# Kernel tuning notes

Measured on AMD Instinct MI355X. Metric: run time of the kernel, lower is better.

## Reference

```python
import jax, jax.numpy as jnp
import numpy as np

N_NODES = 10000
AVG_DEG = 32
N_FEAT = 512
HIDDEN = 32
CODE = 16


def setup_inputs() -> dict:
    key = jax.random.key(0)
    k1, k2, k3, k4, k5 = jax.random.split(key, 5)
    E = N_NODES * AVG_DEG
    src = jax.random.randint(k1, (E,), 0, N_NODES, dtype=jnp.int32)
    dst = jax.random.randint(k2, (E,), 0, N_NODES, dtype=jnp.int32)
    # A + I: add self loops (Kipf & Welling transform)
    loop = jnp.arange(N_NODES, dtype=jnp.int32)
    src = jnp.concatenate([src, loop])
    dst = jnp.concatenate([dst, loop])
    ones = jnp.ones(src.shape[0], jnp.float32)
    deg_row = jax.ops.segment_sum(ones, dst, num_segments=N_NODES)
    deg_col = jax.ops.segment_sum(ones, src, num_segments=N_NODES)
    # symmetric normalization D^-1/2 (A+I) D^-1/2
    edge_weight = jax.lax.rsqrt(deg_row[dst] * deg_col[src])
    x = jax.random.normal(k3, (N_NODES, N_FEAT), dtype=jnp.float32)
    W1 = jax.random.normal(k4, (N_FEAT, HIDDEN), dtype=jnp.float32) * 0.1
    W2 = jax.random.normal(k5, (HIDDEN, CODE), dtype=jnp.float32) * 0.1
    return {"x": x, "W1": W1, "W2": W2, "edge_weight": edge_weight,
            "src": src, "dst": dst}


def _spmm(edge_weight, src, dst, X):
    # sparse A_hat @ X via gather + weighted scatter-add
    return jax.ops.segment_sum(edge_weight[:, None] * X[src], dst,
                               num_segments=X.shape[0])


def reference(x, W1, W2, edge_weight, src, dst):
    # layer 1: A_hat @ (x @ W1), relu  (dropout inactive: eval mode)
    h = jax.nn.relu(_spmm(edge_weight, src, dst, x @ W1))
    # layer 2 (encoder): A_hat @ (h @ W2)
    z = _spmm(edge_weight, src, dst, h @ W2)  # [N, code]
    # inner-product decoder: sigmoid(Z Z^T)
    return jax.nn.sigmoid(jnp.einsum('nc,mc->nm', z, z))
```

## Files before the change

### kernel.cpp

```cpp
#include <hip/hip_runtime.h>
#include <hip/hip_bf16.h>

#define N_NODES 10000
#define N_FEAT  512
#define HIDDEN  32
#define CODE    16

typedef __attribute__((ext_vector_type(8))) short  short8;
typedef __attribute__((ext_vector_type(4))) float  floatx4;

__device__ __forceinline__ float bf2f(unsigned short h) {
    return __uint_as_float(((unsigned int)h) << 16);
}
__device__ __forceinline__ unsigned short f2bf(float f) {
    unsigned int u = __float_as_uint(f);
    u += 0x7fffu + ((u >> 16) & 1u);
    return (unsigned short)(u >> 16);
}
__device__ __forceinline__ float load_f(const void* p, size_t i, int isf32) {
    return isf32 ? ((const float*)p)[i] : bf2f(((const unsigned short*)p)[i]);
}
__device__ __forceinline__ int get_idx(const int* p, int e, int is64) {
    return is64 ? p[2 * (size_t)e] : p[e];
}

__global__ __launch_bounds__(384) void k_detect(const unsigned short* __restrict__ t0,
                                                const unsigned short* __restrict__ t1,
                                                const unsigned short* __restrict__ t2,
                                                const unsigned short* __restrict__ t3,
                                                const int* __restrict__ i0,
                                                const int* __restrict__ i1,
                                                int* __restrict__ flags) {
    const int w    = threadIdx.x >> 6;
    const int lane = threadIdx.x & 63;
    unsigned int m = 0;
    if (w < 4) {
        const unsigned short* p = (w == 0) ? t0 : (w == 1) ? t1 : (w == 2) ? t2 : t3;
        for (int i = lane; i < 128; i += 64) {
            unsigned int v = (unsigned int)p[2 * i] & 0x7fffu;
            m = m > v ? m : v;
        }
    } else {
        const int* p = (w == 4) ? i0 : i1;
        for (int i = lane; i < 128; i += 64) {
            m |= (unsigned int)p[2 * i + 1];
        }
    }
#pragma unroll
    for (int off = 32; off > 0; off >>= 1) {
        unsigned int o = (unsigned int)__shfl_down((int)m, off, 64);
        m = (w < 4) ? (m > o ? m : o) : (m | o);
    }
    if (lane == 0) flags[w] = (w < 4) ? (m >= 0x5000u ? 1 : 0) : (m == 0u ? 1 : 0);
}

__global__ __launch_bounds__(256) void k_xw1(const void* __restrict__ x,
                                             const void* __restrict__ W1,
                                             float* __restrict__ XW1,
                                             const int* __restrict__ flags) {
    const int xf32  = flags[0];
    const int w1f32 = flags[1];
    int t = blockIdx.x * 256 + threadIdx.x;
    if (t >= N_NODES * HIDDEN) return;
    const int n = t >> 5;
    const int c = t & 31;
    float acc = 0.f;
#pragma unroll 8
    for (int k = 0; k < N_FEAT; ++k) {
        float a = load_f(x,  (size_t)n * N_FEAT + k, xf32);
        float b = load_f(W1, (size_t)k * HIDDEN + c, w1f32);
        acc += a * b;
    }
    XW1[t] = acc;
}

__global__ __launch_bounds__(256) void k_spmm32(const void* __restrict__ ew,
                                                const int* __restrict__ src,
                                                const int* __restrict__ dst,
                                                const float* __restrict__ Xin,
                                                float* __restrict__ Hacc, int E,
                                                const int* __restrict__ flags) {
    const int ewf32 = flags[3];
    const int s64   = flags[4];
    const int d64   = flags[5];
    int t = blockIdx.x * 256 + threadIdx.x;
    int e = t >> 5;
    int f = t & 31;
    if (e >= E) return;
    float w = load_f(ew, e, ewf32);
    int   s = get_idx(src, e, s64);
    int   d = get_idx(dst, e, d64);
    float v = Xin[(size_t)s * HIDDEN + f] * w;
    atomicAdd(&Hacc[(size_t)d * HIDDEN + f], v);
}

__global__ __launch_bounds__(256) void k_hw2(const float* __restrict__ H,
                                             const void* __restrict__ W2,
                                             float* __restrict__ HW2,
                                             const int* __restrict__ flags) {
    const int w2f32 = flags[2];
    int t = blockIdx.x * 256 + threadIdx.x;
    if (t >= N_NODES * CODE) return;
    int n = t >> 4;
    int c = t & 15;
    float acc = 0.f;
#pragma unroll
    for (int k = 0; k < HIDDEN; ++k) {
        float h = H[n * HIDDEN + k];
        h = h > 0.f ? h : 0.f;
        acc += h * load_f(W2, k * CODE + c, w2f32);
    }
    HW2[t] = acc;
}

__global__ __launch_bounds__(256) void k_spmm16(const void* __restrict__ ew,
                                                const int* __restrict__ src,
                                                const int* __restrict__ dst,
                                                const float* __restrict__ Hin,
                                                float* __restrict__ Zacc, int E,
                                                const int* __restrict__ flags) {
    const int ewf32 = flags[3];
    const int s64   = flags[4];
    const int d64   = flags[5];
    int t = blockIdx.x * 256 + threadIdx.x;
    int e = t >> 4;
    int f = t & 15;
    if (e >= E) return;
    float w = load_f(ew, e, ewf32);
    int   s = get_idx(src, e, s64);
    int   d = get_idx(dst, e, d64);
    float v = Hin[(size_t)s * CODE + f] * w;
    atomicAdd(&Zacc[(size_t)d * CODE + f], v);
}

__global__ __launch_bounds__(256) void k_cvt(const float* __restrict__ Z,
                                             unsigned short* __restrict__ zb) {
    int t = blockIdx.x * 256 + threadIdx.x;
    if (t >= N_NODES * CODE) return;
    zb[t] = f2bf(Z[t]);
}

__global__ __launch_bounds__(256) void k_dec(const unsigned short* __restrict__ zb,
                                             float* __restrict__ out) {
    const int wave = threadIdx.x >> 6;
    const int lane = threadIdx.x & 63;
    const int l16  = lane & 15;
    const int quad = lane >> 4;

    const int r0 = blockIdx.y * 64 + wave * 16;
    const int c0 = blockIdx.x * 64;

    const short8 zero8 = {0, 0, 0, 0, 0, 0, 0, 0};

    int ra = r0 + l16;
    if (ra > N_NODES - 1) ra = N_NODES - 1;
    short8 afr = zero8;
    if (quad < 2) afr = *(const short8*)(zb + (size_t)ra * CODE + quad * 8);

    floatx4 acc[4];
#pragma unroll
    for (int t = 0; t < 4; ++t) {
        int cb = c0 + t * 16 + l16;
        if (cb > N_NODES - 1) cb = N_NODES - 1;
        short8 bfr = zero8;
        if (quad < 2) bfr = *(const short8*)(zb + (size_t)cb * CODE + quad * 8);
        floatx4 z4 = {0.f, 0.f, 0.f, 0.f};
        acc[t] = __builtin_amdgcn_mfma_f32_16x16x32_bf16(afr, bfr, z4, 0, 0, 0);
    }

#pragma unroll
    for (int t = 0; t < 4; ++t) {
        const int row  = c0 + t * 16 + l16;
        const int colb = r0 + quad * 4;
        floatx4 v;
#pragma unroll
        for (int r = 0; r < 4; ++r) {
            float s = acc[t][r];
            float e = __builtin_amdgcn_exp2f(-1.442695041f * s);
            v[r] = __builtin_amdgcn_rcpf(1.f + e);
        }
        if (row < N_NODES && colb < N_NODES) {
            __builtin_nontemporal_store(v, (floatx4*)(out + (size_t)row * N_NODES + colb));
        }
    }
}

extern "C" void kernel_launch(void* const* d_in, const int* in_sizes, int n_in,
                              void* d_out, int out_size, void* d_ws, size_t ws_size,
                              hipStream_t stream) {
    const void* x  = d_in[0];
    const void* W1 = d_in[1];
    const void* W2 = d_in[2];
    const void* ew = d_in[3];
    const int* src = (const int*)d_in[4];
    const int* dst = (const int*)d_in[5];
    float* out = (float*)d_out;
    const int E = in_sizes[3];

    float* ws   = (float*)d_ws;
    float* XW1  = ws;
    float* Hacc = ws + 320000;
    float* HW2  = ws;
    float* Zacc = ws + 160000;
    unsigned short* zb = (unsigned short*)(ws + 320000);
    int* flags = (int*)(ws + 640000);

    hipMemsetAsync(Hacc, 0, 320000 * sizeof(float), stream);

    k_detect<<<1, 384, 0, stream>>>((const unsigned short*)x,
                                    (const unsigned short*)W1,
                                    (const unsigned short*)W2,
                                    (const unsigned short*)ew,
                                    src, dst, flags);

    k_xw1<<<(N_NODES * HIDDEN + 255) / 256, 256, 0, stream>>>(x, W1, XW1, flags);
    k_spmm32<<<(E * 32 + 255) / 256, 256, 0, stream>>>(ew, src, dst, XW1, Hacc, E, flags);
    hipMemsetAsync(Zacc, 0, 160000 * sizeof(float), stream);
    k_hw2<<<(N_NODES * CODE + 255) / 256, 256, 0, stream>>>(Hacc, W2, HW2, flags);
    k_spmm16<<<(E * 16 + 255) / 256, 256, 0, stream>>>(ew, src, dst, HW2, Zacc, E, flags);
    k_cvt<<<(N_NODES * CODE + 255) / 256, 256, 0, stream>>>(Zacc, zb);

    dim3 grid((N_NODES + 63) / 64, (N_NODES + 63) / 64);
    k_dec<<<grid, 256, 0, stream>>>(zb, out);
}
```

Baseline: 589.9 us.

## Stage decoder tile through LDS for row-contiguous stores; vectorize fp32 XW1 path

The decoder now writes each MFMA result into a padded shared-memory tile, then re-reads it so each thread emits contiguous float4 stores along output rows. The aim is coalesced writes of the 400 MB output, which dominates runtime. The old layout scattered 16-byte stores across rows. The cost is an LDS round trip and a block barrier. Separately, the XW1 kernel gets an fp32 fast path that reads x as float4 vectors.

```diff
diff --git a/kernel.cpp b/kernel.cpp
--- a/kernel.cpp
+++ b/kernel.cpp
@@ -64,6 +64,23 @@
     if (t >= N_NODES * HIDDEN) return;
     const int n = t >> 5;
     const int c = t & 31;
+
+    if (xf32 && w1f32) {
+        const float* xr = (const float*)x + (size_t)n * N_FEAT;
+        const float* w1 = (const float*)W1;
+        float acc = 0.f;
+#pragma unroll 4
+        for (int k = 0; k < N_FEAT; k += 4) {
+            floatx4 xa = *(const floatx4*)(xr + k);
+            acc += xa[0] * w1[(k + 0) * HIDDEN + c];
+            acc += xa[1] * w1[(k + 1) * HIDDEN + c];
+            acc += xa[2] * w1[(k + 2) * HIDDEN + c];
+            acc += xa[3] * w1[(k + 3) * HIDDEN + c];
+        }
+        XW1[t] = acc;
+        return;
+    }
+
     float acc = 0.f;
 #pragma unroll 8
     for (int k = 0; k < N_FEAT; ++k) {
@@ -140,15 +157,20 @@
     zb[t] = f2bf(Z[t]);
 }
 
+#define TLD 68
+
 __global__ __launch_bounds__(256) void k_dec(const unsigned short* __restrict__ zb,
                                              float* __restrict__ out) {
+    __shared__ float tile[64 * TLD];
+
     const int wave = threadIdx.x >> 6;
     const int lane = threadIdx.x & 63;
     const int l16  = lane & 15;
     const int quad = lane >> 4;
 
-    const int r0 = blockIdx.y * 64 + wave * 16;
-    const int c0 = blockIdx.x * 64;
+    const int rblk = blockIdx.y * 64;
+    const int cblk = blockIdx.x * 64;
+    const int r0   = rblk + wave * 16;
 
     const short8 zero8 = {0, 0, 0, 0, 0, 0, 0, 0};
 
@@ -157,30 +179,39 @@
     short8 afr = zero8;
     if (quad < 2) afr = *(const short8*)(zb + (size_t)ra * CODE + quad * 8);
 
-    floatx4 acc[4];
 #pragma unroll
     for (int t = 0; t < 4; ++t) {
-        int cb = c0 + t * 16 + l16;
+        int cb = cblk + t * 16 + l16;
         if (cb > N_NODES - 1) cb = N_NODES - 1;
         short8 bfr = zero8;
         if (quad < 2) bfr = *(const short8*)(zb + (size_t)cb * CODE + quad * 8);
         floatx4 z4 = {0.f, 0.f, 0.f, 0.f};
-        acc[t] = __builtin_amdgcn_mfma_f32_16x16x32_bf16(afr, bfr, z4, 0, 0, 0);
-    }
-
-#pragma unroll
-    for (int t = 0; t < 4; ++t) {
-        const int row  = c0 + t * 16 + l16;
-        const int colb = r0 + quad * 4;
+        floatx4 acc = __builtin_amdgcn_mfma_f32_16x16x32_bf16(afr, bfr, z4, 0, 0, 0);
+        const int lrow = wave * 16 + quad * 4;
+        const int lcol = t * 16 + l16;
+#pragma unroll
+        for (int r = 0; r < 4; ++r) {
+            tile[(lrow + r) * TLD + lcol] = acc[r];
+        }
+    }
+    __syncthreads();
+
+    const int drow = threadIdx.x >> 4;
+    const int dcol = (threadIdx.x & 15) * 4;
+#pragma unroll
+    for (int p = 0; p < 4; ++p) {
+        const int lr = p * 16 + drow;
         floatx4 v;
 #pragma unroll
-        for (int r = 0; r < 4; ++r) {
-            float s = acc[t][r];
+        for (int j = 0; j < 4; ++j) {
+            float s = tile[lr * TLD + dcol + j];
             float e = __builtin_amdgcn_exp2f(-1.442695041f * s);
-            v[r] = __builtin_amdgcn_rcpf(1.f + e);
-        }
-        if (row < N_NODES && colb < N_NODES) {
-            __builtin_nontemporal_store(v, (floatx4*)(out + (size_t)row * N_NODES + colb));
+            v[j] = __builtin_amdgcn_rcpf(1.f + e);
+        }
+        const int grow = rblk + lr;
+        const int gcol = cblk + dcol;
+        if (grow < N_NODES && gcol < N_NODES) {
+            __builtin_nontemporal_store(v, (floatx4*)(out + (size_t)grow * N_NODES + gcol));
         }
     }
 }
```

New measurement: 528.0 us. -10.5%, faster.
